# Performance work log

Measured on AMD Instinct MI355X. Metric: run time of the kernel, lower is better.

## Reference

```python
import jax, jax.numpy as jnp
import numpy as np

N = 50000      # nodes
E = 1600000    # edges
F = 128        # num_feature
H = 256        # num_hidden
L = 3          # num_message_passing_steps
EPS = 1e-5     # LayerNorm eps (torch default)


def setup_inputs() -> dict:
    key = jax.random.key(0)
    ks = jax.random.split(key, 8)
    node = jax.random.normal(ks[0], (N, F), dtype=jnp.float32)
    edges = jax.random.randint(ks[1], (2, E), 0, N, dtype=jnp.int64)
    edges_attr = jax.random.uniform(ks[2], (E,), dtype=jnp.float32)
    sF = np.float32(1.0 / np.sqrt(F))
    sH = np.float32(1.0 / np.sqrt(H))
    W1 = jax.random.normal(ks[3], (F, H), dtype=jnp.float32) * sF
    b1 = jnp.zeros((H,), jnp.float32)
    W_convs = jax.random.normal(ks[4], (L, H, H), dtype=jnp.float32) * sH
    b_convs = jnp.zeros((L, H), jnp.float32)
    ln_g = jnp.ones((L, H), jnp.float32)
    ln_b = jnp.zeros((L, H), jnp.float32)
    fc_W = jax.random.normal(ks[5], (H, 2), dtype=jnp.float32) * sH
    fc_b = jnp.zeros((2,), jnp.float32)
    return dict(node=node, edges=edges, edges_attr=edges_attr, W1=W1, b1=b1,
                W_convs=W_convs, b_convs=b_convs, ln_g=ln_g, ln_b=ln_b,
                fc_W=fc_W, fc_b=fc_b)


def gcn_conv(x, src_a, dst_a, w_a, W, b):
    # PyG GCNConv: x' = D^-1/2 (A + I) D^-1/2 (x W) + b, edge weights w.
    # src_a/dst_a/w_a already include self-loops (weight 1).
    n = x.shape[0]
    xw = x @ W                                      # [N, H]
    deg = jax.ops.segment_sum(w_a, dst_a, num_segments=n)
    deg_safe = jnp.where(deg > 0, deg, 1.0)
    dinv = jnp.where(deg > 0, jax.lax.rsqrt(deg_safe), 0.0)
    norm = dinv[src_a] * w_a * dinv[dst_a]          # [E+N]
    msg = xw[src_a] * norm[:, None]                 # gather + scale
    out = jax.ops.segment_sum(msg, dst_a, num_segments=n)  # scatter-add
    return out + b


def layer_norm(x, g, b):
    mu = jnp.mean(x, axis=-1, keepdims=True)
    var = jnp.mean((x - mu) ** 2, axis=-1, keepdims=True)
    return (x - mu) * jax.lax.rsqrt(var + EPS) * g + b


def reference(node, edges, edges_attr, W1, b1, W_convs, b_convs, ln_g, ln_b, fc_W, fc_b):
    n = node.shape[0]
    loop = jnp.arange(n, dtype=edges.dtype)
    src_a = jnp.concatenate([edges[0], loop])
    dst_a = jnp.concatenate([edges[1], loop])
    w_a = jnp.concatenate([edges_attr, jnp.ones((n,), edges_attr.dtype)])

    x = gcn_conv(node, src_a, dst_a, w_a, W1, b1)
    for i in range(L):
        x_res = x
        x = gcn_conv(x, src_a, dst_a, w_a, W_convs[i], b_convs[i])
        x = layer_norm(x, ln_g[i], ln_b[i])
        x = jax.nn.relu(x + x_res)
    x = x @ fc_W + fc_b                              # [N, 2]
    return jnp.mean(x, axis=0, keepdims=True)        # global_mean_pool, batch=None -> [1, 2]
```

## Files before the change

kernel.cpp:

```cpp
#include <hip/hip_runtime.h>

#define EPS 1e-5f
#define FIXSCALE 8388608.0f
#define NBK 64

typedef __attribute__((ext_vector_type(8))) short short8;
typedef __attribute__((ext_vector_type(4))) short short4v;
typedef __attribute__((ext_vector_type(4))) float float4v;
typedef __attribute__((ext_vector_type(2))) float float2v;
typedef __attribute__((ext_vector_type(8))) unsigned short ushort8;
typedef __attribute__((ext_vector_type(4))) unsigned int uint4v;

#if __has_builtin(__builtin_nontemporal_load)
#define NT_LOAD(p) __builtin_nontemporal_load(p)
#else
#define NT_LOAD(p) (*(p))
#endif

__device__ __forceinline__ unsigned short f2b(float f) {
    union { float f; unsigned u; } v; v.f = f;
    unsigned r = v.u + 0x7FFF + ((v.u >> 16) & 1);
    return (unsigned short)(r >> 16);
}
__device__ __forceinline__ float b2f(unsigned short u) {
    union { unsigned u; float f; } v; v.u = ((unsigned)u) << 16;
    return v.f;
}

__device__ __forceinline__ int qbucket(int cnt) {
    int qc = ((cnt + 4) & ~3) >> 2;
    return qc < NBK - 1 ? qc : NBK - 1;
}


__global__ __launch_bounds__(256) void rank_kernel(const int* __restrict__ dst,
                                                   const float* __restrict__ w,
                                                   unsigned long long* __restrict__ combo,
                                                   int* __restrict__ rank, int E) {
    int e = blockIdx.x * 256 + threadIdx.x;
    if (e < E) {
        int d = dst[e];
        unsigned long long pack = (1ULL << 32) | (unsigned long long)(unsigned)(w[e] * FIXSCALE);
        unsigned long long old = atomicAdd(&combo[(size_t)d * 8], pack);
        rank[e] = (int)(old >> 32);
    }
}

__global__ __launch_bounds__(256) void dinv_kernel(const unsigned long long* __restrict__ combo,
                                                   float* __restrict__ dinv, int n) {
    int d = blockIdx.x * 256 + threadIdx.x;
    if (d < n) {
        float degv = (float)(unsigned)(combo[(size_t)d * 8] & 0xffffffffULL) * (1.0f / FIXSCALE);
        dinv[d] = rsqrtf(degv + 1.0f);
    }
}


__global__ __launch_bounds__(256) void bin_hist_kernel(const unsigned long long* __restrict__ combo,
                                                       int* __restrict__ blockhist, int n) {
    __shared__ int lh[NBK];
    int t = threadIdx.x;
    if (t < NBK) lh[t] = 0;
    __syncthreads();
    int d = blockIdx.x * 256 + t;
    if (d < n) {
        int cnt = (int)(combo[(size_t)d * 8] >> 32);
        atomicAdd(&lh[qbucket(cnt)], 1);
    }
    __syncthreads();
    if (t < NBK) blockhist[blockIdx.x * NBK + t] = lh[t];
}

__global__ __launch_bounds__(256) void bin_prescan_kernel(const int* __restrict__ blockhist,
                                                          int* __restrict__ blockpre,
                                                          int* __restrict__ tot, int nblk) {
    int bkt = blockIdx.x;
    int t = threadIdx.x, lane = t & 63, w = t >> 6;
    __shared__ int wsum[4];
    __shared__ int s_carry;
    if (t == 0) s_carry = 0;
    __syncthreads();
    for (int base = 0; base < nblk; base += 256) {
        int i = base + t;
        int v = (i < nblk) ? blockhist[i * NBK + bkt] : 0;
        int x = v;
        for (int off = 1; off < 64; off <<= 1) {
            int u = __shfl_up(x, off);
            if (lane >= off) x += u;
        }
        if (lane == 63) wsum[w] = x;
        __syncthreads();
        if (t == 0) {
            int a = wsum[0];
            wsum[0] = 0;
            for (int k = 1; k < 4; ++k) { int b = wsum[k]; wsum[k] = a; a += b; }
            wsum[0] = 0;
        }
        __syncthreads();
        int carry = s_carry;
        int woff = wsum[w];
        if (i < nblk) blockpre[i * NBK + bkt] = carry + woff + x - v;
        __syncthreads();
        if (t == 255) s_carry = carry + woff + x;
        __syncthreads();
    }
    if (t == 0) tot[bkt] = s_carry;
}

__global__ __launch_bounds__(64) void bin_suffix_kernel(const int* __restrict__ tot,
                                                        int* __restrict__ base) {
    int t = threadIdx.x;
    int v = tot[t];
    int s = v;
    for (int off = 1; off < 64; off <<= 1) {
        int u = __shfl_down(s, off);
        if (t + off < 64) s += u;
    }
    base[t] = s - v;
}

__global__ __launch_bounds__(256) void bin_scatter_kernel(const unsigned long long* __restrict__ combo,
                                                          const int* __restrict__ base,
                                                          const int* __restrict__ blockpre,
                                                          int* __restrict__ perm,
                                                          int* __restrict__ posod,
                                                          int* __restrict__ qlen, int n) {
    __shared__ int lcur[NBK];
    int t = threadIdx.x;
    if (t < NBK) lcur[t] = base[t] + blockpre[blockIdx.x * NBK + t];
    __syncthreads();
    int d = blockIdx.x * 256 + t;
    if (d < n) {
        int cnt = (int)(combo[(size_t)d * 8] >> 32);
        int pos = atomicAdd(&lcur[qbucket(cnt)], 1);
        perm[pos] = d;
        posod[d] = pos;
        qlen[pos] = (cnt + 4) & ~3;
    }
}

__global__ __launch_bounds__(1024) void scan_kernel(const int* __restrict__ qlen,
                                                    int* __restrict__ row_ptr, int n) {
    int tid = threadIdx.x, lane = tid & 63, w = tid >> 6;
    __shared__ int wsum[16];
    __shared__ int s_carry;
    if (tid == 0) s_carry = 0;
    __syncthreads();
    for (int base = 0; base < n; base += 1024) {
        int i = base + tid;
        int v = (i < n) ? qlen[i] : 0;
        int x = v;
        for (int off = 1; off < 64; off <<= 1) {
            int t = __shfl_up(x, off);
            if (lane >= off) x += t;
        }
        if (lane == 63) wsum[w] = x;
        __syncthreads();
        if (w == 0 && lane < 16) {
            int s = wsum[lane];
            for (int off = 1; off < 16; off <<= 1) {
                int t = __shfl_up(s, off, 16);
                if (lane >= off) s += t;
            }
            wsum[lane] = s;
        }
        __syncthreads();
        int carry = s_carry;
        int woff = (w > 0) ? wsum[w - 1] : 0;
        if (i < n) row_ptr[i + 1] = carry + woff + x;
        __syncthreads();
        if (tid == 0) s_carry = carry + wsum[15];
        __syncthreads();
    }
    if (tid == 0) row_ptr[0] = 0;
}

__global__ __launch_bounds__(256) void selfpad_kernel(const unsigned long long* __restrict__ combo,
                                                      const int* __restrict__ row_ptr,
                                                      const int* __restrict__ posod,
                                                      const float* __restrict__ dinv,
                                                      unsigned int* __restrict__ edge, int n) {
    int d = blockIdx.x * 256 + threadIdx.x;
    if (d < n) {
        int cnt = (int)(combo[(size_t)d * 8] >> 32);
        int slot = posod[d];
        int j0 = row_ptr[slot], j1 = row_ptr[slot + 1];
        float di = dinv[d];
        edge[j0] = ((unsigned)f2b(di * di) << 16) | (unsigned)slot;
        for (int j = j0 + 1 + cnt; j < j1; ++j) edge[j] = (unsigned)slot;
    }
}

__global__ __launch_bounds__(256) void scatter2_kernel(
    const int* __restrict__ src, const int* __restrict__ dst,
    const float* __restrict__ w, const int* __restrict__ rank,
    const int* __restrict__ row_ptr, const int* __restrict__ posod,
    const float* __restrict__ dinv, unsigned int* __restrict__ edge, int E) {
    int e = blockIdx.x * 256 + threadIdx.x;
    if (e < E) {
        int d = dst[e], s = src[e];
        float wn = dinv[s] * w[e] * dinv[d];
        edge[row_ptr[posod[d]] + 1 + rank[e]] = ((unsigned)f2b(wn) << 16) | (unsigned)posod[s];
    }
}

__global__ __launch_bounds__(256) void cast_sliced_kernel(const float* __restrict__ in,
                                                          const int* __restrict__ perm,
                                                          unsigned short* __restrict__ out,
                                                          int n, int F) {
    int idx = blockIdx.x * 256 + threadIdx.x;
    if (idx < n * (F / 4)) {
        int f4 = idx * 4;
        int slot = f4 / F, f = f4 - slot * F;
        float4 v = *(const float4*)&in[(size_t)perm[slot] * F + f];
        short4v s = (short4v){(short)f2b(v.x), (short)f2b(v.y), (short)f2b(v.z), (short)f2b(v.w)};
        *(short4v*)&out[((size_t)(f >> 5) * n + slot) * 32 + (f & 31)] = s;
    }
}

__global__ __launch_bounds__(256) void wtrans_kernel(const float* __restrict__ W,
                                                     unsigned short* __restrict__ Wt,
                                                     int K, int Nc) {
    int o = blockIdx.x * 256 + threadIdx.x;
    if (o < K * Nc) {
        int n = o / K, k = o - n * K;
        Wt[o] = f2b(W[(size_t)k * Nc + n]);
    }
}


#define GST 88

template <bool SLICEOUT>
__global__ __launch_bounds__(256) void gemm_n256(const unsigned short* __restrict__ A,
                                                 const unsigned short* __restrict__ Bt,
                                                 unsigned short* __restrict__ Cout,
                                                 const float* __restrict__ bias,
                                                 int M, int K) {
    __shared__ __align__(16) short As[64 * GST];
    __shared__ __align__(16) short Bs[256 * GST];
    int t = threadIdx.x;
    int lane = t & 63, w = t >> 6;
    int quad = lane >> 4, l16 = lane & 15;
    int row0 = blockIdx.x * 64;

    float4v acc[16];
#pragma unroll
    for (int c = 0; c < 16; ++c) acc[c] = (float4v){0.f, 0.f, 0.f, 0.f};

    int arow = t >> 2, ak16 = (t & 3) * 16;
    int bcol0 = t >> 2, bko = (t & 3) * 16;

    for (int k_outer = 0; k_outer < K; k_outer += 64) {
        bool rowok = (row0 + arow) < M;
        const unsigned short* ap = &A[(size_t)(row0 + arow) * K + k_outer + ak16];
        uint4 z = make_uint4(0, 0, 0, 0);
        uint4 u0 = rowok ? *(const uint4*)ap : z;
        uint4 u1 = rowok ? *(const uint4*)(ap + 8) : z;
        *(uint4*)&As[arow * GST + ak16] = u0;
        *(uint4*)&As[arow * GST + ak16 + 8] = u1;
#pragma unroll
        for (int cb = 0; cb < 4; ++cb) {
            int col = bcol0 + 64 * cb;
            const unsigned short* bp = &Bt[(size_t)col * K + k_outer + bko];
#pragma unroll
            for (int u = 0; u < 2; ++u)
                *(uint4*)&Bs[col * GST + bko + u * 8] = *(const uint4*)&bp[u * 8];
        }
        __syncthreads();
#pragma unroll
        for (int k0 = 0; k0 < 64; k0 += 32) {
            short8 a = *(const short8*)&As[(w * 16 + l16) * GST + k0 + quad * 8];
#pragma unroll
            for (int c = 0; c < 16; ++c) {
                short8 b = *(const short8*)&Bs[(c * 16 + l16) * GST + k0 + quad * 8];
                acc[c] = __builtin_amdgcn_mfma_f32_16x16x32_bf16(a, b, acc[c], 0, 0, 0);
            }
        }
        __syncthreads();
    }
#pragma unroll
    for (int c = 0; c < 16; ++c) {
        int col = c * 16 + l16;
        float bcol = (!SLICEOUT) ? bias[col] : 0.0f;
#pragma unroll
        for (int r = 0; r < 4; ++r) {
            int row = row0 + w * 16 + quad * 4 + r;
            if (row < M) {
                if (SLICEOUT)
                    Cout[((size_t)(c >> 1) * M + row) * 32 + ((c & 1) << 4) + l16] = f2b(acc[c][r]);
                else
                    Cout[(size_t)row * 256 + col] = f2b(acc[c][r] + bcol);
            }
        }
    }
}


#define CAPQ 1024

template <int CSH>
__global__ __launch_bounds__(256) void agg_grp(
    const unsigned short* __restrict__ tab0, const int* __restrict__ row_ptr,
    const unsigned int* __restrict__ edge, unsigned short* __restrict__ outb, int n) {
    __shared__ uint4v eq[CAPQ];
    int b = blockIdx.x;
    int s = b & ((1 << CSH) - 1);
    int grp = b >> CSH;
    int t = threadIdx.x;
    int d0 = grp * 64;
    int d = d0 + (t >> 2);

    const uint4v* e4p = (const uint4v*)edge;
    int qbase = row_ptr[d0] >> 2;
    int dmax = d0 + 64 < n ? d0 + 64 : n;
    int qcnt = (row_ptr[dmax] >> 2) - qbase;
    int qstage = qcnt < CAPQ ? qcnt : CAPQ;
    for (int i = t; i < qstage; i += 256) eq[i] = NT_LOAD(&e4p[qbase + i]);
    __syncthreads();

    if (d >= n) return;
    int fo = (t & 3) << 3;
    const unsigned short* tab = tab0 + (size_t)s * n * 32;

    int j = row_ptr[d] >> 2, j1 = row_ptr[d + 1] >> 2;
    int jmid = j1 < qbase + CAPQ ? j1 : qbase + CAPQ;

    float2v a2[4];
#pragma unroll
    for (int k = 0; k < 4; ++k) a2[k] = (float2v){0.f, 0.f};

    auto process = [&](uint4v e4) {
#pragma unroll
        for (int u = 0; u < 4; ++u) {
            unsigned e = e4[u];
            float wq = __int_as_float((int)(e & 0xffff0000u));
            float2v w2 = {wq, wq};
            unsigned off = ((e & 0xffffu) << 5) + (unsigned)fo;
            uint4 rr = *(const uint4*)(tab + off);
            unsigned uu0 = rr.x, uu1 = rr.y, uu2 = rr.z, uu3 = rr.w;
            float2v f0 = {__uint_as_float(uu0 << 16), __uint_as_float(uu0 & 0xffff0000u)};
            float2v f1 = {__uint_as_float(uu1 << 16), __uint_as_float(uu1 & 0xffff0000u)};
            float2v f2 = {__uint_as_float(uu2 << 16), __uint_as_float(uu2 & 0xffff0000u)};
            float2v f3 = {__uint_as_float(uu3 << 16), __uint_as_float(uu3 & 0xffff0000u)};
            a2[0] += f0 * w2;
            a2[1] += f1 * w2;
            a2[2] += f2 * w2;
            a2[3] += f3 * w2;
        }
    };

    for (; j + 2 <= jmid; j += 2) {
        uint4v e4a = eq[j - qbase];
        uint4v e4b = eq[j + 1 - qbase];
        process(e4a);
        process(e4b);
    }
    if (j < jmid) { process(eq[j - qbase]); ++j; }
    for (; j < j1; ++j) process(NT_LOAD(&e4p[j]));

    ushort8 o;
#pragma unroll
    for (int k = 0; k < 4; ++k) {
        o[2 * k] = f2b(a2[k].x);
        o[2 * k + 1] = f2b(a2[k].y);
    }
    *(ushort8*)(outb + ((size_t)d << (5 + CSH)) + (s << 5) + fo) = o;
}


__global__ __launch_bounds__(256) void ln_res_relu(
    const unsigned short* __restrict__ preln, const float* __restrict__ bias,
    const float* __restrict__ g, const float* __restrict__ lb,
    const unsigned short* __restrict__ res, unsigned short* __restrict__ out, int n) {
    int wv = __builtin_amdgcn_readfirstlane(threadIdx.x >> 6);
    int d = blockIdx.x * 4 + wv;
    if (d >= n) return;
    int l = threadIdx.x & 63;
    int fo = l * 4;
    ushort4 pv = *(const ushort4*)&preln[(size_t)d * 256 + fo];
    float4 bb = *(const float4*)&bias[fo];
    float v[4] = {b2f(pv.x) + bb.x, b2f(pv.y) + bb.y, b2f(pv.z) + bb.z, b2f(pv.w) + bb.w};
    float s4 = v[0] + v[1] + v[2] + v[3];
#pragma unroll
    for (int off = 1; off < 64; off <<= 1) s4 += __shfl_xor(s4, off);
    float mu = s4 * (1.0f / 256.0f);
    float dv[4];
    float qs = 0.f;
#pragma unroll
    for (int j = 0; j < 4; ++j) { dv[j] = v[j] - mu; qs += dv[j] * dv[j]; }
#pragma unroll
    for (int off = 1; off < 64; off <<= 1) qs += __shfl_xor(qs, off);
    float rs = rsqrtf(qs * (1.0f / 256.0f) + EPS);

    float4 gg = *(const float4*)&g[fo];
    float4 lbv = *(const float4*)&lb[fo];
    ushort4 rr4 = *(const ushort4*)&res[(size_t)d * 256 + fo];
    float ggv[4] = {gg.x, gg.y, gg.z, gg.w};
    float lbvv[4] = {lbv.x, lbv.y, lbv.z, lbv.w};
    float rrv[4] = {b2f(rr4.x), b2f(rr4.y), b2f(rr4.z), b2f(rr4.w)};
    ushort4 o;
    unsigned short* op = (unsigned short*)&o;
#pragma unroll
    for (int j = 0; j < 4; ++j) {
        float x = dv[j] * rs * ggv[j] + lbvv[j] + rrv[j];
        op[j] = f2b(x > 0.f ? x : 0.f);
    }
    *(ushort4*)&out[(size_t)d * 256 + fo] = o;
}


__global__ __launch_bounds__(256) void colsum_kernel(const unsigned short* __restrict__ x,
                                                     float* __restrict__ sums, int n) {
    int h = threadIdx.x;
    float acc = 0.0f;
    for (int r = blockIdx.x; r < n; r += gridDim.x) acc += b2f(x[(size_t)r * 256 + h]);
    atomicAdd(&sums[h], acc);
}

__global__ __launch_bounds__(64) void final_kernel(const float* __restrict__ sums,
                                                   const float* __restrict__ fcW,
                                                   const float* __restrict__ fcb,
                                                   float* __restrict__ out, float invN) {
    int lane = threadIdx.x;
    float p0 = 0.0f, p1 = 0.0f;
    for (int hh = lane; hh < 256; hh += 64) {
        float m = sums[hh];
        p0 += m * fcW[hh * 2 + 0];
        p1 += m * fcW[hh * 2 + 1];
    }
    for (int off = 32; off > 0; off >>= 1) {
        p0 += __shfl_down(p0, off);
        p1 += __shfl_down(p1, off);
    }
    if (lane == 0) {
        out[0] = p0 * invN + fcb[0];
        out[1] = p1 * invN + fcb[1];
    }
}


extern "C" void kernel_launch(void* const* d_in, const int* in_sizes, int n_in,
                              void* d_out, int out_size, void* d_ws, size_t ws_size,
                              hipStream_t stream) {
    const float* node    = (const float*)d_in[0];
    const int*   edges   = (const int*)d_in[1];
    const float* eattr   = (const float*)d_in[2];
    const float* W1      = (const float*)d_in[3];
    const float* b1      = (const float*)d_in[4];
    const float* W_convs = (const float*)d_in[5];
    const float* b_convs = (const float*)d_in[6];
    const float* ln_g    = (const float*)d_in[7];
    const float* ln_b    = (const float*)d_in[8];
    const float* fc_W    = (const float*)d_in[9];
    const float* fc_b    = (const float*)d_in[10];
    float* out = (float*)d_out;

    const int H = in_sizes[4];
    const int F = in_sizes[3] / H;
    const int N = in_sizes[0] / F;
    const int E = in_sizes[2];
    const int L = in_sizes[6] / H;

    const int* src = edges;
    const int* dst = edges + E;

    char* p = (char*)d_ws;
    auto alloc = [&](size_t bytes) {
        char* r = p;
        p += (bytes + 255) & ~(size_t)255;
        return r;
    };
    int nblk = (N + 255) / 256;
    unsigned long long* combo = (unsigned long long*)alloc((size_t)N * 64);
    float* colsums = (float*)alloc((size_t)H * 4);
    size_t zero_bytes = (size_t)((char*)colsums - (char*)combo) + (((size_t)H * 4 + 255) & ~(size_t)255);
    int*   blockhist = (int*)alloc((size_t)nblk * NBK * 4);
    int*   blockpre  = (int*)alloc((size_t)nblk * NBK * 4);
    int*   tot       = (int*)alloc((size_t)NBK * 4);
    int*   bbase     = (int*)alloc((size_t)NBK * 4);
    int*   perm    = (int*)alloc((size_t)N * 4);
    int*   posod   = (int*)alloc((size_t)N * 4);
    int*   qlen    = (int*)alloc((size_t)N * 4);
    float* dinv    = (float*)alloc((size_t)N * 4);
    int*   row_ptr = (int*)alloc((size_t)(N + 1) * 4);
    unsigned int* edge = (unsigned int*)alloc(((size_t)E + 4 * (size_t)N + 64) * 4);
    unsigned short* Wt1 = (unsigned short*)alloc((size_t)H * F * 2);
    unsigned short* Wtc = (unsigned short*)alloc((size_t)L * H * H * 2);
    unsigned short* xw  = (unsigned short*)alloc((size_t)N * H * 2);
    unsigned short* preln = (unsigned short*)alloc((size_t)N * H * 2);
    unsigned short* bufA  = (unsigned short*)alloc((size_t)N * H * 2);
    unsigned short* bufB  = (unsigned short*)alloc((size_t)N * H * 2);
    int*            rank  = (int*)xw;
    unsigned short* nodeb = preln;
    unsigned short* aggn  = preln + (size_t)N * F;

    hipMemsetAsync(combo, 0, zero_bytes, stream);

    int gE = (E + 255) / 256;
    rank_kernel<<<gE, 256, 0, stream>>>(dst, eattr, combo, rank, E);
    dinv_kernel<<<nblk, 256, 0, stream>>>(combo, dinv, N);
    bin_hist_kernel<<<nblk, 256, 0, stream>>>(combo, blockhist, N);
    bin_prescan_kernel<<<NBK, 256, 0, stream>>>(blockhist, blockpre, tot, nblk);
    bin_suffix_kernel<<<1, 64, 0, stream>>>(tot, bbase);
    bin_scatter_kernel<<<nblk, 256, 0, stream>>>(combo, bbase, blockpre, perm, posod, qlen, N);
    scan_kernel<<<1, 1024, 0, stream>>>(qlen, row_ptr, N);
    selfpad_kernel<<<nblk, 256, 0, stream>>>(combo, row_ptr, posod, dinv, edge, N);
    scatter2_kernel<<<gE, 256, 0, stream>>>(src, dst, eattr, rank, row_ptr, posod, dinv, edge, E);

    cast_sliced_kernel<<<(N * (F / 4) + 255) / 256, 256, 0, stream>>>(node, perm, nodeb, N, F);
    wtrans_kernel<<<(F * H + 255) / 256, 256, 0, stream>>>(W1, Wt1, F, H);
    for (int i = 0; i < L; ++i)
        wtrans_kernel<<<(H * H + 255) / 256, 256, 0, stream>>>(
            W_convs + (size_t)i * H * H, Wtc + (size_t)i * H * H, H, H);

    int ngrp64 = (N + 63) / 64;
    int lngrid = (N + 3) / 4;
    int ggrid = (N + 63) / 64;

    agg_grp<2><<<4 * ngrp64, 256, 0, stream>>>(nodeb, row_ptr, edge, aggn, N);
    gemm_n256<false><<<ggrid, 256, 0, stream>>>(aggn, Wt1, bufA, b1, N, F);

    unsigned short* x = bufA;
    unsigned short* other = bufB;
    for (int i = 0; i < L; ++i) {
        gemm_n256<true><<<ggrid, 256, 0, stream>>>(x, Wtc + (size_t)i * H * H, xw, nullptr, N, H);
        agg_grp<3><<<8 * ngrp64, 256, 0, stream>>>(xw, row_ptr, edge, preln, N);
        ln_res_relu<<<lngrid, 256, 0, stream>>>(preln, b_convs + (size_t)i * H,
                                                ln_g + (size_t)i * H, ln_b + (size_t)i * H,
                                                x, other, N);
        unsigned short* t = x; x = other; other = t;
    }

    colsum_kernel<<<256, 256, 0, stream>>>(x, colsums, N);
    final_kernel<<<1, 64, 0, stream>>>(colsums, fc_W, fc_b, out, 1.0f / (float)N);
}
```

Baseline: 729.8 us.

## Merge dinv and histogram kernels, parallelize row-pointer scan, batch weight transposes

Fuses the degree-inverse computation into the bucket histogram kernel so combo is read once and one launch is dropped. Replaces the single-block serial prefix scan over N node lengths with a three-stage multi-block scan (local, mid, add). Merges the three per-layer weight transpose launches into one. These target launch overhead and the serial scan in preprocessing, which is small next to the GEMM and aggregation work.

```diff
diff --git a/kernel.cpp b/kernel.cpp
--- a/kernel.cpp
+++ b/kernel.cpp
@@ -46,25 +46,19 @@
     }
 }
 
-__global__ __launch_bounds__(256) void dinv_kernel(const unsigned long long* __restrict__ combo,
-                                                   float* __restrict__ dinv, int n) {
-    int d = blockIdx.x * 256 + threadIdx.x;
-    if (d < n) {
-        float degv = (float)(unsigned)(combo[(size_t)d * 8] & 0xffffffffULL) * (1.0f / FIXSCALE);
-        dinv[d] = rsqrtf(degv + 1.0f);
-    }
-}
-
-
-__global__ __launch_bounds__(256) void bin_hist_kernel(const unsigned long long* __restrict__ combo,
-                                                       int* __restrict__ blockhist, int n) {
+__global__ __launch_bounds__(256) void dinv_hist_kernel(const unsigned long long* __restrict__ combo,
+                                                        float* __restrict__ dinv,
+                                                        int* __restrict__ blockhist, int n) {
     __shared__ int lh[NBK];
     int t = threadIdx.x;
     if (t < NBK) lh[t] = 0;
     __syncthreads();
     int d = blockIdx.x * 256 + t;
     if (d < n) {
-        int cnt = (int)(combo[(size_t)d * 8] >> 32);
+        unsigned long long cw = combo[(size_t)d * 8];
+        int cnt = (int)(cw >> 32);
+        float degv = (float)(unsigned)(cw & 0xffffffffULL) * (1.0f / FIXSCALE);
+        dinv[d] = rsqrtf(degv + 1.0f);
         atomicAdd(&lh[qbucket(cnt)], 1);
     }
     __syncthreads();
@@ -139,40 +133,57 @@
     }
 }
 
-__global__ __launch_bounds__(1024) void scan_kernel(const int* __restrict__ qlen,
-                                                    int* __restrict__ row_ptr, int n) {
+
+__global__ __launch_bounds__(1024) void scan_local_kernel(const int* __restrict__ qlen,
+                                                          int* __restrict__ row_ptr,
+                                                          int* __restrict__ bsum, int n) {
     int tid = threadIdx.x, lane = tid & 63, w = tid >> 6;
     __shared__ int wsum[16];
-    __shared__ int s_carry;
-    if (tid == 0) s_carry = 0;
-    __syncthreads();
-    for (int base = 0; base < n; base += 1024) {
-        int i = base + tid;
-        int v = (i < n) ? qlen[i] : 0;
+    int i = blockIdx.x * 1024 + tid;
+    int v = (i < n) ? qlen[i] : 0;
+    int x = v;
+    for (int off = 1; off < 64; off <<= 1) {
+        int t = __shfl_up(x, off);
+        if (lane >= off) x += t;
+    }
+    if (lane == 63) wsum[w] = x;
+    __syncthreads();
+    if (w == 0 && lane < 16) {
+        int s = wsum[lane];
+        for (int off = 1; off < 16; off <<= 1) {
+            int t = __shfl_up(s, off, 16);
+            if (lane >= off) s += t;
+        }
+        wsum[lane] = s;
+    }
+    __syncthreads();
+    int woff = (w > 0) ? wsum[w - 1] : 0;
+    if (i < n) row_ptr[i + 1] = woff + x;
+    if (tid == 0) bsum[blockIdx.x] = wsum[15];
+}
+
+__global__ __launch_bounds__(64) void scan_mid_kernel(int* __restrict__ bsum,
+                                                      int* __restrict__ row_ptr, int nb) {
+    int t = threadIdx.x;
+    int carry = 0;
+    for (int base = 0; base < nb; base += 64) {
+        int idx = base + t;
+        int v = (idx < nb) ? bsum[idx] : 0;
         int x = v;
         for (int off = 1; off < 64; off <<= 1) {
-            int t = __shfl_up(x, off);
-            if (lane >= off) x += t;
-        }
-        if (lane == 63) wsum[w] = x;
-        __syncthreads();
-        if (w == 0 && lane < 16) {
-            int s = wsum[lane];
-            for (int off = 1; off < 16; off <<= 1) {
-                int t = __shfl_up(s, off, 16);
-                if (lane >= off) s += t;
-            }
-            wsum[lane] = s;
-        }
-        __syncthreads();
-        int carry = s_carry;
-        int woff = (w > 0) ? wsum[w - 1] : 0;
-        if (i < n) row_ptr[i + 1] = carry + woff + x;
-        __syncthreads();
-        if (tid == 0) s_carry = carry + wsum[15];
-        __syncthreads();
-    }
-    if (tid == 0) row_ptr[0] = 0;
+            int u = __shfl_up(x, off);
+            if (t >= off) x += u;
+        }
+        if (idx < nb) bsum[idx] = carry + x - v;
+        carry += __shfl(x, 63);
+    }
+    if (t == 0) row_ptr[0] = 0;
+}
+
+__global__ __launch_bounds__(1024) void scan_add_kernel(const int* __restrict__ bsum,
+                                                        int* __restrict__ row_ptr, int n) {
+    int i = blockIdx.x * 1024 + threadIdx.x;
+    if (i < n) row_ptr[i + 1] += bsum[blockIdx.x];
 }
 
 __global__ __launch_bounds__(256) void selfpad_kernel(const unsigned long long* __restrict__ combo,
@@ -218,13 +229,15 @@
     }
 }
 
-__global__ __launch_bounds__(256) void wtrans_kernel(const float* __restrict__ W,
-                                                     unsigned short* __restrict__ Wt,
-                                                     int K, int Nc) {
+__global__ __launch_bounds__(256) void wtransL_kernel(const float* __restrict__ W,
+                                                      unsigned short* __restrict__ Wt,
+                                                      int K, int Nc, int total) {
     int o = blockIdx.x * 256 + threadIdx.x;
-    if (o < K * Nc) {
-        int n = o / K, k = o - n * K;
-        Wt[o] = f2b(W[(size_t)k * Nc + n]);
+    if (o < total) {
+        int l = o / (K * Nc);
+        int r = o - l * K * Nc;
+        int n = r / K, k = r - n * K;
+        Wt[o] = f2b(W[(size_t)l * K * Nc + (size_t)k * Nc + n]);
     }
 }
 
@@ -472,6 +485,7 @@
         return r;
     };
     int nblk = (N + 255) / 256;
+    int nb1024 = (N + 1023) / 1024;
     unsigned long long* combo = (unsigned long long*)alloc((size_t)N * 64);
     float* colsums = (float*)alloc((size_t)H * 4);
     size_t zero_bytes = (size_t)((char*)colsums - (char*)combo) + (((size_t)H * 4 + 255) & ~(size_t)255);
@@ -484,6 +498,7 @@
     int*   qlen    = (int*)alloc((size_t)N * 4);
     float* dinv    = (float*)alloc((size_t)N * 4);
     int*   row_ptr = (int*)alloc((size_t)(N + 1) * 4);
+    int*   bsum    = (int*)alloc((size_t)nb1024 * 4);
     unsigned int* edge = (unsigned int*)alloc(((size_t)E + 4 * (size_t)N + 64) * 4);
     unsigned short* Wt1 = (unsigned short*)alloc((size_t)H * F * 2);
     unsigned short* Wtc = (unsigned short*)alloc((size_t)L * H * H * 2);
@@ -499,20 +514,19 @@
 
     int gE = (E + 255) / 256;
     rank_kernel<<<gE, 256, 0, stream>>>(dst, eattr, combo, rank, E);
-    dinv_kernel<<<nblk, 256, 0, stream>>>(combo, dinv, N);
-    bin_hist_kernel<<<nblk, 256, 0, stream>>>(combo, blockhist, N);
+    dinv_hist_kernel<<<nblk, 256, 0, stream>>>(combo, dinv, blockhist, N);
     bin_prescan_kernel<<<NBK, 256, 0, stream>>>(blockhist, blockpre, tot, nblk);
     bin_suffix_kernel<<<1, 64, 0, stream>>>(tot, bbase);
     bin_scatter_kernel<<<nblk, 256, 0, stream>>>(combo, bbase, blockpre, perm, posod, qlen, N);
-    scan_kernel<<<1, 1024, 0, stream>>>(qlen, row_ptr, N);
+    scan_local_kernel<<<nb1024, 1024, 0, stream>>>(qlen, row_ptr, bsum, N);
+    scan_mid_kernel<<<1, 64, 0, stream>>>(bsum, row_ptr, nb1024);
+    scan_add_kernel<<<nb1024, 1024, 0, stream>>>(bsum, row_ptr, N);
     selfpad_kernel<<<nblk, 256, 0, stream>>>(combo, row_ptr, posod, dinv, edge, N);
     scatter2_kernel<<<gE, 256, 0, stream>>>(src, dst, eattr, rank, row_ptr, posod, dinv, edge, E);
 
     cast_sliced_kernel<<<(N * (F / 4) + 255) / 256, 256, 0, stream>>>(node, perm, nodeb, N, F);
-    wtrans_kernel<<<(F * H + 255) / 256, 256, 0, stream>>>(W1, Wt1, F, H);
-    for (int i = 0; i < L; ++i)
-        wtrans_kernel<<<(H * H + 255) / 256, 256, 0, stream>>>(
-            W_convs + (size_t)i * H * H, Wtc + (size_t)i * H * H, H, H);
+    wtransL_kernel<<<(F * H + 255) / 256, 256, 0, stream>>>(W1, Wt1, F, H, F * H);
+    wtransL_kernel<<<(L * H * H + 255) / 256, 256, 0, stream>>>(W_convs, Wtc, H, H, L * H * H);
 
     int ngrp64 = (N + 63) / 64;
     int lngrid = (N + 3) / 4;
```

Measured after the change: 693.5 us. -5.0%, faster.
